# Performance work log

Measured on AMD Instinct MI355X. Metric: run time of the kernel, lower is better.

## Reference

```python
import jax, jax.numpy as jnp
import numpy as np

N_NODES = 20000
N_EDGES = 320000
HIDDEN = 256
N_GRAPHS = 64
IN_DIM = 3
OUT_DIM = 2


def _glorot(key, shape):
    fan_in, fan_out = shape
    lim = jnp.sqrt(6.0 / (fan_in + fan_out))
    return jax.random.uniform(key, shape, jnp.float32, -lim, lim)


def setup_inputs() -> dict:
    key = jax.random.key(0)
    ks = jax.random.split(key, 16)
    inp = {
        "x": jax.random.normal(ks[0], (N_NODES, IN_DIM), jnp.float32),
        "edge_index": jax.random.randint(ks[1], (2, N_EDGES), 0, N_NODES, jnp.int64),
        "batch": jnp.sort(jax.random.randint(ks[2], (N_NODES,), 0, N_GRAPHS, jnp.int64)),
        "W1": _glorot(ks[3], (IN_DIM, HIDDEN)), "b1": jnp.zeros((HIDDEN,), jnp.float32),
        "W2": _glorot(ks[4], (HIDDEN, HIDDEN)), "b2": jnp.zeros((HIDDEN,), jnp.float32),
        "W3": _glorot(ks[5], (HIDDEN, HIDDEN)), "b3": jnp.zeros((HIDDEN,), jnp.float32),
        "W4": _glorot(ks[6], (HIDDEN, HIDDEN)), "b4": jnp.zeros((HIDDEN,), jnp.float32),
        "W5": _glorot(ks[7], (HIDDEN, HIDDEN)), "b5": jnp.zeros((HIDDEN,), jnp.float32),
        "Wlin": _glorot(ks[8], (HIDDEN, OUT_DIM)), "blin": jnp.zeros((OUT_DIM,), jnp.float32),
    }
    return inp


def _gcn_norm(edge_index, n_nodes):
    # PyG GCNConv default: add self-loops, symmetric degree normalization.
    loops = jnp.arange(n_nodes, dtype=edge_index.dtype)
    src = jnp.concatenate([edge_index[0], loops])
    dst = jnp.concatenate([edge_index[1], loops])
    deg = jax.ops.segment_sum(jnp.ones_like(dst, jnp.float32), dst, num_segments=n_nodes)
    dinv = jnp.where(deg > 0, jax.lax.rsqrt(deg), 0.0)
    norm = dinv[src] * dinv[dst]  # [E + N]
    return src, dst, norm


def _gcn_layer(x, W, b, src, dst, norm, n_nodes):
    h = x @ W                                   # [N, H]
    msg = h[src] * norm[:, None]                # [E+N, H] gather + scale
    agg = jax.ops.segment_sum(msg, dst, num_segments=n_nodes)  # scatter-add
    return agg + b


def reference(x, edge_index, batch, W1, b1, W2, b2, W3, b3, W4, b4, W5, b5, Wlin, blin):
    n = x.shape[0]
    src, dst, norm = _gcn_norm(edge_index, n)
    h = jax.nn.relu(_gcn_layer(x, W1, b1, src, dst, norm, n))
    h = jax.nn.relu(_gcn_layer(h, W2, b2, src, dst, norm, n))
    h = jax.nn.relu(_gcn_layer(h, W3, b3, src, dst, norm, n))
    h = jax.nn.relu(_gcn_layer(h, W4, b4, src, dst, norm, n))
    h = jax.nn.relu(_gcn_layer(h, W5, b5, src, dst, norm, n))
    pooled = jax.ops.segment_sum(h, batch, num_segments=N_GRAPHS)  # global_add_pool
    return pooled @ Wlin + blin
```

## Files before the change

### kernel.cpp

```cpp
#include <hip/hip_runtime.h>

#define N_NODES 20000
#define N_PAD 20096
#define N_EDGES 320000
#define HIDDEN 256
#define N_GRAPHS 64
#define OUT_DIM 2

#define QPANEL_BYTES 65536
#define QTABLE_BYTES 32768
#define GEMM_GRID 628

typedef __attribute__((ext_vector_type(8))) short short8v;
typedef __attribute__((ext_vector_type(4))) float f32x4;
typedef __attribute__((ext_vector_type(4))) unsigned short us4;

__global__ void k_degree(const int* __restrict__ dst, int* __restrict__ degi) {
    int e = blockIdx.x * blockDim.x + threadIdx.x;
    if (e < N_EDGES) atomicAdd(&degi[dst[e]], 1);
}

__global__ void k_scan(const int* __restrict__ degi, int* __restrict__ rowptr,
                       int* __restrict__ rowstart, float* __restrict__ dinv) {
    __shared__ int sums[1024];
    int t = threadIdx.x;
    int base = t * 20;
    int ld[20];
    int local = 0;
    if (t < 1000) {
#pragma unroll
        for (int i = 0; i < 20; ++i) {
            ld[i] = degi[base + i];
            local += ld[i];
            dinv[base + i] = rsqrtf((float)ld[i] + 1.0f);
        }
    }
    sums[t] = local;
    __syncthreads();
    for (int off = 1; off < 1024; off <<= 1) {
        int v = (t >= off) ? sums[t - off] : 0;
        __syncthreads();
        sums[t] += v;
        __syncthreads();
    }
    if (t < 1000) {
        int run = (t == 0) ? 0 : sums[t - 1];
#pragma unroll
        for (int i = 0; i < 20; ++i) {
            rowptr[base + i] = run;
            rowstart[base + i] = run;
            run += ld[i];
        }
    }
    if (t == 1023) rowptr[N_NODES] = sums[1023];
}

__global__ void k_fill(const int* __restrict__ src, const int* __restrict__ dst,
                       const float* __restrict__ dinv, int* __restrict__ rowstart,
                       int2* __restrict__ csr) {
    int e = blockIdx.x * blockDim.x + threadIdx.x;
    if (e >= N_EDGES) return;
    int s = src[e], d = dst[e];
    int pos = atomicAdd(&rowstart[d], 1);
    csr[pos] = make_int2(s, __float_as_int(dinv[s] * dinv[d]));
}

__global__ void k_wprep4(const float* __restrict__ W2, const float* __restrict__ W3,
                         const float* __restrict__ W4, const float* __restrict__ W5,
                         char* __restrict__ wt) {
    int lid = blockIdx.x >> 8;
    int idx = (blockIdx.x & 255) * 256 + threadIdx.x;
    const float* W = lid == 0 ? W2 : lid == 1 ? W3 : lid == 2 ? W4 : W5;
    int k = idx & 255, n = idx >> 8;
    float a = W[k * 256 + n];
    unsigned u = __float_as_uint(a);
    ushort hi = (ushort)(u >> 16);
    float hif = __uint_as_float(u & 0xffff0000u);
    ushort lo = (ushort)(__float_as_uint(a - hif) >> 16);
    int q = n >> 6, colQ = n & 63, slab = k >> 3, e = k & 7;
    size_t base = ((size_t)lid * 4 + q) * QPANEL_BYTES;
    size_t soff = (size_t)slab * 1024 + ((colQ * 16 + slab * 32) & 1023) + e * 2;
    *(ushort*)(wt + base + soff) = hi;
    *(ushort*)(wt + base + QTABLE_BYTES + soff) = lo;
}

__global__ void k_aggx(const float* __restrict__ x, const float* __restrict__ dinv,
                       const int* __restrict__ rowptr, const int2* __restrict__ csr,
                       float* __restrict__ z) {
    int t = blockIdx.x * blockDim.x + threadIdx.x;
    int i = t >> 2, c = t & 3;
    if (i >= N_NODES || c >= 3) return;
    float di = dinv[i];
    float a = di * di * x[i * 3 + c], bacc = 0.f;
    int k = rowptr[i], end = rowptr[i + 1];
    for (; k + 1 < end; k += 2) {
        int2 e0 = csr[k], e1 = csr[k + 1];
        a = fmaf(x[(size_t)e0.x * 3 + c], __int_as_float(e0.y), a);
        bacc = fmaf(x[(size_t)e1.x * 3 + c], __int_as_float(e1.y), bacc);
    }
    if (k < end) {
        int2 e0 = csr[k];
        a = fmaf(x[(size_t)e0.x * 3 + c], __int_as_float(e0.y), a);
    }
    z[i * 3 + c] = a + bacc;
}

__global__ void k_h1(const float* __restrict__ z, const float* __restrict__ W1,
                     const float* __restrict__ b1,
                     ushort* __restrict__ out_hi, ushort* __restrict__ out_lo) {
    int i = blockIdx.x;
    int j = threadIdx.x;
    float z0 = z[i * 3], z1 = z[i * 3 + 1], z2 = z[i * 3 + 2];
    float v = fmaf(z0, W1[j], fmaf(z1, W1[256 + j], fmaf(z2, W1[512 + j], b1[j])));
    v = fmaxf(v, 0.0f);
    unsigned u = __float_as_uint(v);
    ushort hi = (ushort)(u >> 16);
    float hif = __uint_as_float(u & 0xffff0000u);
    ushort lo = (ushort)(__float_as_uint(v - hif) >> 16);
    out_hi[(size_t)i * HIDDEN + j] = hi;
    out_lo[(size_t)i * HIDDEN + j] = lo;
}

__global__ void k_csr_agg(const float* __restrict__ h, const float* __restrict__ dinv,
                          const int* __restrict__ rowptr, const int2* __restrict__ csr,
                          const float* __restrict__ b,
                          ushort* __restrict__ out_hi, ushort* __restrict__ out_lo) {
    int node = blockIdx.x * 4 + (threadIdx.x >> 6);
    if (node >= N_NODES) return;
    int lane = threadIdx.x & 63;
    int beg = rowptr[node], end = rowptr[node + 1];
    float di = dinv[node];
    float w0 = di * di;
    float4 bv = *reinterpret_cast<const float4*>(b + lane * 4);
    float4 hv = *reinterpret_cast<const float4*>(h + (size_t)node * HIDDEN + lane * 4);
    float4 A0, A1 = {0,0,0,0}, A2 = {0,0,0,0}, A3 = {0,0,0,0};
    A0.x = fmaf(hv.x, w0, bv.x);
    A0.y = fmaf(hv.y, w0, bv.y);
    A0.z = fmaf(hv.z, w0, bv.z);
    A0.w = fmaf(hv.w, w0, bv.w);
    int k = beg;
    for (; k + 3 < end; k += 4) {
        int2 e0 = csr[k], e1 = csr[k + 1], e2 = csr[k + 2], e3 = csr[k + 3];
        float we0 = __int_as_float(e0.y), we1 = __int_as_float(e1.y);
        float we2 = __int_as_float(e2.y), we3 = __int_as_float(e3.y);
        float4 v0 = *reinterpret_cast<const float4*>(h + (size_t)e0.x * HIDDEN + lane * 4);
        float4 v1 = *reinterpret_cast<const float4*>(h + (size_t)e1.x * HIDDEN + lane * 4);
        float4 v2 = *reinterpret_cast<const float4*>(h + (size_t)e2.x * HIDDEN + lane * 4);
        float4 v3 = *reinterpret_cast<const float4*>(h + (size_t)e3.x * HIDDEN + lane * 4);
        A0.x = fmaf(v0.x, we0, A0.x);  A1.x = fmaf(v1.x, we1, A1.x);
        A0.y = fmaf(v0.y, we0, A0.y);  A1.y = fmaf(v1.y, we1, A1.y);
        A0.z = fmaf(v0.z, we0, A0.z);  A1.z = fmaf(v1.z, we1, A1.z);
        A0.w = fmaf(v0.w, we0, A0.w);  A1.w = fmaf(v1.w, we1, A1.w);
        A2.x = fmaf(v2.x, we2, A2.x);  A3.x = fmaf(v3.x, we3, A3.x);
        A2.y = fmaf(v2.y, we2, A2.y);  A3.y = fmaf(v3.y, we3, A3.y);
        A2.z = fmaf(v2.z, we2, A2.z);  A3.z = fmaf(v3.z, we3, A3.z);
        A2.w = fmaf(v2.w, we2, A2.w);  A3.w = fmaf(v3.w, we3, A3.w);
    }
    for (; k < end; ++k) {
        int2 e0 = csr[k];
        float we0 = __int_as_float(e0.y);
        float4 v0 = *reinterpret_cast<const float4*>(h + (size_t)e0.x * HIDDEN + lane * 4);
        A0.x = fmaf(v0.x, we0, A0.x);
        A0.y = fmaf(v0.y, we0, A0.y);
        A0.z = fmaf(v0.z, we0, A0.z);
        A0.w = fmaf(v0.w, we0, A0.w);
    }
    float4 acc;
    acc.x = (A0.x + A1.x) + (A2.x + A3.x);
    acc.y = (A0.y + A1.y) + (A2.y + A3.y);
    acc.z = (A0.z + A1.z) + (A2.z + A3.z);
    acc.w = (A0.w + A1.w) + (A2.w + A3.w);
    float rv[4] = {fmaxf(acc.x, 0.f), fmaxf(acc.y, 0.f), fmaxf(acc.z, 0.f), fmaxf(acc.w, 0.f)};
    us4 hvv, lvv;
#pragma unroll
    for (int j = 0; j < 4; ++j) {
        unsigned u = __float_as_uint(rv[j]);
        hvv[j] = (ushort)(u >> 16);
        float hif = __uint_as_float(u & 0xffff0000u);
        lvv[j] = (ushort)(__float_as_uint(rv[j] - hif) >> 16);
    }
    *reinterpret_cast<us4*>(out_hi + (size_t)node * HIDDEN + lane * 4) = hvv;
    *reinterpret_cast<us4*>(out_lo + (size_t)node * HIDDEN + lane * 4) = lvv;
}

__global__ __launch_bounds__(512) void k_gemm_mfma(const ushort* __restrict__ a_hi,
                                                   const ushort* __restrict__ a_lo,
                                                   const char* __restrict__ wpanels,
                                                   float* __restrict__ out) {
    __shared__ char smem[QPANEL_BYTES];
    int d = blockIdx.x;
    int xcd = d & 7, idx = d >> 3;
    const int q0 = GEMM_GRID / 8, r = GEMM_GRID % 8;
    int base = xcd * q0 + (xcd < r ? xcd : r);
    int logical = base + idx;
    int mtile = logical >> 2, q = logical & 3;

    const char* gsrc = wpanels + (size_t)q * QPANEL_BYTES;
    int tid = threadIdx.x;
#pragma unroll
    for (int it = 0; it < 8; ++it) {
        int o = it * 8192 + tid * 16;
        *reinterpret_cast<float4*>(smem + o) = *reinterpret_cast<const float4*>(gsrc + o);
    }
    __syncthreads();

    int w = tid >> 6, l = tid & 63;
    int lr = l & 15, kg = l >> 4;
    int wm = w >> 1, wn = w & 1;
    int row0 = mtile * 128 + wm * 32;
    int colQ0 = wn * 32;

    const ushort* aph = a_hi + (size_t)(row0 + lr) * HIDDEN + kg * 8;
    const ushort* apl = a_lo + (size_t)(row0 + lr) * HIDDEN + kg * 8;

    short8v ah0 = *reinterpret_cast<const short8v*>(aph);
    short8v ah1 = *reinterpret_cast<const short8v*>(aph + 16 * HIDDEN);
    short8v al0 = *reinterpret_cast<const short8v*>(apl);
    short8v al1 = *reinterpret_cast<const short8v*>(apl + 16 * HIDDEN);

    f32x4 acc[2][2] = {};
#pragma unroll
    for (int t = 0; t < 8; ++t) {
        short8v cah0 = ah0, cah1 = ah1, cal0 = al0, cal1 = al1;
        if (t < 7) {
            int kb = (t + 1) * 32;
            ah0 = *reinterpret_cast<const short8v*>(aph + kb);
            ah1 = *reinterpret_cast<const short8v*>(aph + 16 * HIDDEN + kb);
            al0 = *reinterpret_cast<const short8v*>(apl + kb);
            al1 = *reinterpret_cast<const short8v*>(apl + 16 * HIDDEN + kb);
        }
        int slab = t * 4 + kg;
        int sbase = slab * 1024;
        int rot = slab * 32;
        int off0 = sbase + (((colQ0 + lr) * 16 + rot) & 1023);
        int off1 = sbase + (((colQ0 + 16 + lr) * 16 + rot) & 1023);
        short8v bh0 = *reinterpret_cast<const short8v*>(smem + off0);
        short8v bh1 = *reinterpret_cast<const short8v*>(smem + off1);
        short8v bl0 = *reinterpret_cast<const short8v*>(smem + QTABLE_BYTES + off0);
        short8v bl1 = *reinterpret_cast<const short8v*>(smem + QTABLE_BYTES + off1);
        acc[0][0] = __builtin_amdgcn_mfma_f32_16x16x32_bf16(cah0, bh0, acc[0][0], 0, 0, 0);
        acc[1][0] = __builtin_amdgcn_mfma_f32_16x16x32_bf16(cah1, bh0, acc[1][0], 0, 0, 0);
        acc[0][1] = __builtin_amdgcn_mfma_f32_16x16x32_bf16(cah0, bh1, acc[0][1], 0, 0, 0);
        acc[1][1] = __builtin_amdgcn_mfma_f32_16x16x32_bf16(cah1, bh1, acc[1][1], 0, 0, 0);
        acc[0][0] = __builtin_amdgcn_mfma_f32_16x16x32_bf16(cal0, bh0, acc[0][0], 0, 0, 0);
        acc[1][0] = __builtin_amdgcn_mfma_f32_16x16x32_bf16(cal1, bh0, acc[1][0], 0, 0, 0);
        acc[0][1] = __builtin_amdgcn_mfma_f32_16x16x32_bf16(cal0, bh1, acc[0][1], 0, 0, 0);
        acc[1][1] = __builtin_amdgcn_mfma_f32_16x16x32_bf16(cal1, bh1, acc[1][1], 0, 0, 0);
        acc[0][0] = __builtin_amdgcn_mfma_f32_16x16x32_bf16(cah0, bl0, acc[0][0], 0, 0, 0);
        acc[1][0] = __builtin_amdgcn_mfma_f32_16x16x32_bf16(cah1, bl0, acc[1][0], 0, 0, 0);
        acc[0][1] = __builtin_amdgcn_mfma_f32_16x16x32_bf16(cah0, bl1, acc[0][1], 0, 0, 0);
        acc[1][1] = __builtin_amdgcn_mfma_f32_16x16x32_bf16(cah1, bl1, acc[1][1], 0, 0, 0);
    }
    int gcol = q * 64 + colQ0 + lr;
#pragma unroll
    for (int rf = 0; rf < 2; ++rf) {
        float* o0 = out + (size_t)(row0 + rf * 16 + kg * 4) * HIDDEN + gcol;
#pragma unroll
        for (int rr = 0; rr < 4; ++rr)
#pragma unroll
            for (int cf = 0; cf < 2; ++cf)
                o0[(size_t)rr * HIDDEN + cf * 16] = acc[rf][cf][rr];
    }
}

__global__ void k_pool(const ushort* __restrict__ hi, const ushort* __restrict__ lo,
                       const int* __restrict__ batch, float* __restrict__ pooled) {
    int base = blockIdx.x * 32;
    int j = threadIdx.x;
    float acc = 0.0f;
    int cur = batch[base];
    for (int r = 0; r < 32; ++r) {
        int i = base + r;
        int bg = batch[i];
        if (bg != cur) {
            atomicAdd(&pooled[cur * HIDDEN + j], acc);
            acc = 0.0f;
            cur = bg;
        }
        size_t off = (size_t)i * HIDDEN + j;
        float v = __uint_as_float((unsigned)hi[off] << 16) +
                  __uint_as_float((unsigned)lo[off] << 16);
        acc += v;
    }
    atomicAdd(&pooled[cur * HIDDEN + j], acc);
}

__global__ void k_final(const float* __restrict__ pooled, const float* __restrict__ Wlin,
                        const float* __restrict__ blin, float* __restrict__ out) {
    int t = threadIdx.x;
    int g = t >> 1, o = t & 1;
    float s = blin[o];
    for (int k = 0; k < HIDDEN; ++k) s += pooled[g * HIDDEN + k] * Wlin[k * OUT_DIM + o];
    out[g * OUT_DIM + o] = s;
}

extern "C" void kernel_launch(void* const* d_in, const int* in_sizes, int n_in,
                              void* d_out, int out_size, void* d_ws, size_t ws_size,
                              hipStream_t stream) {
    const float* x     = (const float*)d_in[0];
    const int*   esrc  = (const int*)d_in[1];
    const int*   edst  = esrc + N_EDGES;
    const int*   batch = (const int*)d_in[2];
    const float* W1 = (const float*)d_in[3];
    const float* b1 = (const float*)d_in[4];
    const float* W2 = (const float*)d_in[5];
    const float* b2 = (const float*)d_in[6];
    const float* W3 = (const float*)d_in[7];
    const float* b3 = (const float*)d_in[8];
    const float* W4 = (const float*)d_in[9];
    const float* b4 = (const float*)d_in[10];
    const float* W5 = (const float*)d_in[11];
    const float* b5 = (const float*)d_in[12];
    const float* Wlin = (const float*)d_in[13];
    const float* blin = (const float*)d_in[14];
    float* out = (float*)d_out;

    char* ws = (char*)d_ws;
    size_t off = 0;
    auto alloc = [&](size_t bytes) { size_t o = off; off += (bytes + 255) & ~size_t(255); return (void*)(ws + o); };

    int*    degi     = (int*)alloc(N_NODES * 4);
    float*  dinv     = (float*)alloc(N_NODES * 4);
    int*    rowptr   = (int*)alloc((N_NODES + 1) * 4);
    int*    rowstart = (int*)alloc(N_NODES * 4);
    int2*   csr      = (int2*)alloc((size_t)N_EDGES * 8);
    float*  hA       = (float*)alloc((size_t)N_PAD * HIDDEN * 4);
    ushort* hb_hi    = (ushort*)alloc((size_t)N_PAD * HIDDEN * 2);
    ushort* hb_lo    = (ushort*)alloc((size_t)N_PAD * HIDDEN * 2);
    float*  pooled   = (float*)alloc(N_GRAPHS * HIDDEN * 4);
    char*   wt       = (char*)alloc((size_t)4 * 4 * QPANEL_BYTES);
    float*  z        = (float*)alloc((size_t)N_NODES * 3 * 4);

    hipMemsetAsync(degi, 0, N_NODES * 4, stream);
    hipMemsetAsync(pooled, 0, N_GRAPHS * HIDDEN * 4, stream);

    k_degree<<<(N_EDGES + 255) / 256, 256, 0, stream>>>(edst, degi);
    k_scan<<<1, 1024, 0, stream>>>(degi, rowptr, rowstart, dinv);
    k_fill<<<(N_EDGES + 255) / 256, 256, 0, stream>>>(esrc, edst, dinv, rowstart, csr);
    k_wprep4<<<1024, 256, 0, stream>>>(W2, W3, W4, W5, wt);

    const float* bs[5] = {b1, b2, b3, b4, b5};

    k_aggx<<<(N_NODES * 4 + 255) / 256, 256, 0, stream>>>(x, dinv, rowptr, csr, z);
    k_h1<<<N_NODES, HIDDEN, 0, stream>>>(z, W1, b1, hb_hi, hb_lo);

    for (int l = 1; l < 5; ++l) {
        k_gemm_mfma<<<GEMM_GRID, 512, 0, stream>>>(
            hb_hi, hb_lo, wt + (size_t)(l - 1) * 4 * QPANEL_BYTES, hA);
        k_csr_agg<<<N_NODES / 4, 256, 0, stream>>>(hA, dinv, rowptr, csr, bs[l], hb_hi, hb_lo);
    }

    k_pool<<<N_NODES / 32, HIDDEN, 0, stream>>>(hb_hi, hb_lo, batch, pooled);
    k_final<<<1, 128, 0, stream>>>(pooled, Wlin, blin, out);
}
```

Measured before the change: 385.9 us.

## Split CSR aggregation across column slices and parallel edges with shuffle reduction

The aggregation kernel changes from one wavefront per node covering all 256 columns to eight blocks per node group. Each block covers a 32-column slice, and each wavefront spreads the node's edges across 8 lane groups, which are combined with xor shuffles. This adds memory-level parallelism to the gather and balances uneven degrees. The cost is 128-byte gathers per edge row instead of 1KB, plus the shuffle reduction. Separately, the two hipMemsetAsync calls are replaced by one small zeroing kernel to cut launch overhead.

```diff
diff --git a/kernel.cpp b/kernel.cpp
--- a/kernel.cpp
+++ b/kernel.cpp
@@ -14,6 +14,12 @@
 typedef __attribute__((ext_vector_type(8))) short short8v;
 typedef __attribute__((ext_vector_type(4))) float f32x4;
 typedef __attribute__((ext_vector_type(4))) unsigned short us4;
+
+__global__ void k_zero(int* __restrict__ degi, float* __restrict__ pooled) {
+    int i = blockIdx.x * 256 + threadIdx.x;
+    if (i < N_NODES) degi[i] = 0;
+    if (i < N_GRAPHS * HIDDEN) pooled[i] = 0.f;
+}
 
 __global__ void k_degree(const int* __restrict__ dst, int* __restrict__ degi) {
     int e = blockIdx.x * blockDim.x + threadIdx.x;
@@ -125,62 +131,52 @@
                           const int* __restrict__ rowptr, const int2* __restrict__ csr,
                           const float* __restrict__ b,
                           ushort* __restrict__ out_hi, ushort* __restrict__ out_lo) {
-    int node = blockIdx.x * 4 + (threadIdx.x >> 6);
-    if (node >= N_NODES) return;
+    int bid = blockIdx.x;
+    int slice = bid & 7;
+    int node = (bid >> 3) * 4 + (threadIdx.x >> 6);
     int lane = threadIdx.x & 63;
+    int c = lane & 7;
+    int e8 = lane >> 3;
+    int scol = slice * 32 + c * 4;
     int beg = rowptr[node], end = rowptr[node + 1];
-    float di = dinv[node];
-    float w0 = di * di;
-    float4 bv = *reinterpret_cast<const float4*>(b + lane * 4);
-    float4 hv = *reinterpret_cast<const float4*>(h + (size_t)node * HIDDEN + lane * 4);
-    float4 A0, A1 = {0,0,0,0}, A2 = {0,0,0,0}, A3 = {0,0,0,0};
-    A0.x = fmaf(hv.x, w0, bv.x);
-    A0.y = fmaf(hv.y, w0, bv.y);
-    A0.z = fmaf(hv.z, w0, bv.z);
-    A0.w = fmaf(hv.w, w0, bv.w);
-    int k = beg;
-    for (; k + 3 < end; k += 4) {
-        int2 e0 = csr[k], e1 = csr[k + 1], e2 = csr[k + 2], e3 = csr[k + 3];
-        float we0 = __int_as_float(e0.y), we1 = __int_as_float(e1.y);
-        float we2 = __int_as_float(e2.y), we3 = __int_as_float(e3.y);
-        float4 v0 = *reinterpret_cast<const float4*>(h + (size_t)e0.x * HIDDEN + lane * 4);
-        float4 v1 = *reinterpret_cast<const float4*>(h + (size_t)e1.x * HIDDEN + lane * 4);
-        float4 v2 = *reinterpret_cast<const float4*>(h + (size_t)e2.x * HIDDEN + lane * 4);
-        float4 v3 = *reinterpret_cast<const float4*>(h + (size_t)e3.x * HIDDEN + lane * 4);
-        A0.x = fmaf(v0.x, we0, A0.x);  A1.x = fmaf(v1.x, we1, A1.x);
-        A0.y = fmaf(v0.y, we0, A0.y);  A1.y = fmaf(v1.y, we1, A1.y);
-        A0.z = fmaf(v0.z, we0, A0.z);  A1.z = fmaf(v1.z, we1, A1.z);
-        A0.w = fmaf(v0.w, we0, A0.w);  A1.w = fmaf(v1.w, we1, A1.w);
-        A2.x = fmaf(v2.x, we2, A2.x);  A3.x = fmaf(v3.x, we3, A3.x);
-        A2.y = fmaf(v2.y, we2, A2.y);  A3.y = fmaf(v3.y, we3, A3.y);
-        A2.z = fmaf(v2.z, we2, A2.z);  A3.z = fmaf(v3.z, we3, A3.z);
-        A2.w = fmaf(v2.w, we2, A2.w);  A3.w = fmaf(v3.w, we3, A3.w);
-    }
-    for (; k < end; ++k) {
-        int2 e0 = csr[k];
-        float we0 = __int_as_float(e0.y);
-        float4 v0 = *reinterpret_cast<const float4*>(h + (size_t)e0.x * HIDDEN + lane * 4);
-        A0.x = fmaf(v0.x, we0, A0.x);
-        A0.y = fmaf(v0.y, we0, A0.y);
-        A0.z = fmaf(v0.z, we0, A0.z);
-        A0.w = fmaf(v0.w, we0, A0.w);
-    }
-    float4 acc;
-    acc.x = (A0.x + A1.x) + (A2.x + A3.x);
-    acc.y = (A0.y + A1.y) + (A2.y + A3.y);
-    acc.z = (A0.z + A1.z) + (A2.z + A3.z);
-    acc.w = (A0.w + A1.w) + (A2.w + A3.w);
-    float rv[4] = {fmaxf(acc.x, 0.f), fmaxf(acc.y, 0.f), fmaxf(acc.z, 0.f), fmaxf(acc.w, 0.f)};
-    us4 hvv, lvv;
-#pragma unroll
-    for (int j = 0; j < 4; ++j) {
-        unsigned u = __float_as_uint(rv[j]);
-        hvv[j] = (ushort)(u >> 16);
-        float hif = __uint_as_float(u & 0xffff0000u);
-        lvv[j] = (ushort)(__float_as_uint(rv[j] - hif) >> 16);
-    }
-    *reinterpret_cast<us4*>(out_hi + (size_t)node * HIDDEN + lane * 4) = hvv;
-    *reinterpret_cast<us4*>(out_lo + (size_t)node * HIDDEN + lane * 4) = lvv;
+    float4 acc = {0.f, 0.f, 0.f, 0.f};
+    for (int k = beg + e8; k < end; k += 8) {
+        int2 e = csr[k];
+        float w = __int_as_float(e.y);
+        float4 v = *reinterpret_cast<const float4*>(h + (size_t)e.x * HIDDEN + scol);
+        acc.x = fmaf(v.x, w, acc.x);
+        acc.y = fmaf(v.y, w, acc.y);
+        acc.z = fmaf(v.z, w, acc.z);
+        acc.w = fmaf(v.w, w, acc.w);
+    }
+#pragma unroll
+    for (int d = 8; d < 64; d <<= 1) {
+        acc.x += __shfl_xor(acc.x, d, 64);
+        acc.y += __shfl_xor(acc.y, d, 64);
+        acc.z += __shfl_xor(acc.z, d, 64);
+        acc.w += __shfl_xor(acc.w, d, 64);
+    }
+    if (e8 == 0) {
+        float di = dinv[node];
+        float w0 = di * di;
+        float4 bv = *reinterpret_cast<const float4*>(b + scol);
+        float4 hv = *reinterpret_cast<const float4*>(h + (size_t)node * HIDDEN + scol);
+        float rv[4];
+        rv[0] = fmaxf(fmaf(hv.x, w0, bv.x + acc.x), 0.f);
+        rv[1] = fmaxf(fmaf(hv.y, w0, bv.y + acc.y), 0.f);
+        rv[2] = fmaxf(fmaf(hv.z, w0, bv.z + acc.z), 0.f);
+        rv[3] = fmaxf(fmaf(hv.w, w0, bv.w + acc.w), 0.f);
+        us4 hvv, lvv;
+#pragma unroll
+        for (int j = 0; j < 4; ++j) {
+            unsigned u = __float_as_uint(rv[j]);
+            hvv[j] = (ushort)(u >> 16);
+            float hif = __uint_as_float(u & 0xffff0000u);
+            lvv[j] = (ushort)(__float_as_uint(rv[j] - hif) >> 16);
+        }
+        *reinterpret_cast<us4*>(out_hi + (size_t)node * HIDDEN + scol) = hvv;
+        *reinterpret_cast<us4*>(out_lo + (size_t)node * HIDDEN + scol) = lvv;
+    }
 }
 
 __global__ __launch_bounds__(512) void k_gemm_mfma(const ushort* __restrict__ a_hi,
@@ -331,9 +327,7 @@
     char*   wt       = (char*)alloc((size_t)4 * 4 * QPANEL_BYTES);
     float*  z        = (float*)alloc((size_t)N_NODES * 3 * 4);
 
-    hipMemsetAsync(degi, 0, N_NODES * 4, stream);
-    hipMemsetAsync(pooled, 0, N_GRAPHS * HIDDEN * 4, stream);
-
+    k_zero<<<(N_NODES + 255) / 256, 256, 0, stream>>>(degi, pooled);
     k_degree<<<(N_EDGES + 255) / 256, 256, 0, stream>>>(edst, degi);
     k_scan<<<1, 1024, 0, stream>>>(degi, rowptr, rowstart, dinv);
     k_fill<<<(N_EDGES + 255) / 256, 256, 0, stream>>>(esrc, edst, dinv, rowstart, csr);
@@ -347,7 +341,7 @@
     for (int l = 1; l < 5; ++l) {
         k_gemm_mfma<<<GEMM_GRID, 512, 0, stream>>>(
             hb_hi, hb_lo, wt + (size_t)(l - 1) * 4 * QPANEL_BYTES, hA);
-        k_csr_agg<<<N_NODES / 4, 256, 0, stream>>>(hA, dinv, rowptr, csr, bs[l], hb_hi, hb_lo);
+        k_csr_agg<<<(N_NODES / 4) * 8, 256, 0, stream>>>(hA, dinv, rowptr, csr, bs[l], hb_hi, hb_lo);
     }
 
     k_pool<<<N_NODES / 32, HIDDEN, 0, stream>>>(hb_hi, hb_lo, batch, pooled);
```

Result: slower. 437.9 us (+13.5%).
